# Kernel tuning notes

Measured on AMD Instinct MI355X. Metric: run time of the kernel, lower is better.

## Reference

```python
import jax, jax.numpy as jnp
import numpy as np
import math

NP, MNP, BS, DIM, NH, TOPK, FF = 512, 4096, 8, 256, 8, 32, 2048
HD = DIM // NH
EPS = 1e-5


def _ln(x, w, b):
    mu = jnp.mean(x, axis=-1, keepdims=True)
    var = jnp.mean((x - mu) ** 2, axis=-1, keepdims=True)
    return (x - mu) / jnp.sqrt(var + EPS) * w + b


def _lin(x, w, b):
    return x @ w.T + b


def setup_inputs() -> dict:
    key = jax.random.key(0)
    ks = jax.random.split(key, 16)
    s = 0.02
    d = {
        "tgt": jax.random.normal(ks[0], (NP, BS, DIM), jnp.float32),
        "memory": jax.random.normal(ks[1], (MNP, BS, DIM), jnp.float32),
        "query_pos": jax.random.normal(ks[2], (NP, BS, DIM), jnp.float32),
        "key_pos": jax.random.normal(ks[3], (MNP, BS, DIM), jnp.float32),
        "cw1": jax.random.normal(ks[4], (DIM, DIM), jnp.float32) * s,
        "cb1": jnp.zeros((DIM,), jnp.float32),
        "cw2": jax.random.normal(ks[5], (DIM, DIM), jnp.float32) * s,
        "cb2": jnp.zeros((DIM,), jnp.float32),
        "cw3": jax.random.normal(ks[6], (DIM, DIM), jnp.float32) * s,
        "cb3": jnp.zeros((DIM,), jnp.float32),
        "sa_in_w": jax.random.normal(ks[7], (3 * DIM, DIM), jnp.float32) * s,
        "sa_in_b": jnp.zeros((3 * DIM,), jnp.float32),
        "sa_out_w": jax.random.normal(ks[8], (DIM, DIM), jnp.float32) * s,
        "sa_out_b": jnp.zeros((DIM,), jnp.float32),
        "ln1_w": jnp.ones((DIM,), jnp.float32),
        "ln1_b": jnp.zeros((DIM,), jnp.float32),
        "ln2_w": jnp.ones((DIM,), jnp.float32),
        "ln2_b": jnp.zeros((DIM,), jnp.float32),
        "ln3_w": jnp.ones((DIM,), jnp.float32),
        "ln3_b": jnp.zeros((DIM,), jnp.float32),
        "ff1_w": jax.random.normal(ks[9], (FF, DIM), jnp.float32) * s,
        "ff1_b": jnp.zeros((FF,), jnp.float32),
        "ff2_w": jax.random.normal(ks[10], (DIM, FF), jnp.float32) * s,
        "ff2_b": jnp.zeros((DIM,), jnp.float32),
    }
    return d


def _forward(tgt, memory, query_pos, key_pos,
             cw1, cb1, cw2, cb2, cw3, cb3,
             sa_in_w, sa_in_b, sa_out_w, sa_out_b,
             ln1_w, ln1_b, ln2_w, ln2_b, ln3_w, ln3_b,
             ff1_w, ff1_b, ff2_w, ff2_b):
    npq, bs, dim = tgt.shape
    mnp = memory.shape[0]
    scale = 1.0 / math.sqrt(HD)

    # --- top-k cosine similarity neighbor selection (indices, non-diff) ---
    x = tgt.transpose(1, 0, 2)        # [bs, np, dim]
    m = memory.transpose(1, 0, 2)     # [bs, mnp, dim]
    xn = x / jnp.linalg.norm(x, axis=2, keepdims=True)
    mn = m / jnp.linalg.norm(m, axis=2, keepdims=True)
    sim = jnp.einsum('bnd,bmd->bnm', xn, mn)          # [bs, np, mnp]
    _, rns = jax.lax.top_k(sim, TOPK)                  # [bs, np, topk]

    # --- masked cross attention ---
    qc = (tgt + query_pos).transpose(1, 0, 2)          # [bs, np, dim]
    kc = (memory + key_pos).transpose(1, 0, 2)         # [bs, mnp, dim]
    vc = m
    qh = _lin(qc, cw1, cb1).reshape(bs, npq, NH, HD).transpose(0, 2, 1, 3)   # [bs,nh,np,hd]
    kh = _lin(kc, cw2, cb2).reshape(bs, mnp, NH, HD).transpose(0, 2, 1, 3)   # [bs,nh,mnp,hd]
    vh = _lin(vc, cw3, cb3).reshape(bs, mnp, NH, HD).transpose(0, 2, 1, 3)   # [bs,nh,mnp,hd]
    w = jnp.einsum('bhnd,bhmd->bhnm', qh, kh) * scale                         # [bs,nh,np,mnp]

    b_idx = jnp.arange(bs)[:, None, None]
    n_idx = jnp.arange(npq)[None, :, None]
    mask = jnp.zeros((bs, npq, mnp), w.dtype).at[b_idx, n_idx, rns].set(1.0)  # same for all heads
    mask = mask[:, None, :, :]                                                # [bs,1,np,mnp]
    w = w * mask + (-1e9) * (1.0 - mask)
    w = jax.nn.softmax(w, axis=3)
    cross = jnp.einsum('bhnm,bhmd->bhnd', w, vh).transpose(2, 0, 1, 3).reshape(npq, bs, dim)

    t = _ln(tgt + cross, ln1_w, ln1_b)

    # --- self attention (torch nn.MultiheadAttention, q=k=t+pos, v=t) ---
    wq, wk, wv = sa_in_w[:DIM], sa_in_w[DIM:2 * DIM], sa_in_w[2 * DIM:]
    bq, bk, bv = sa_in_b[:DIM], sa_in_b[DIM:2 * DIM], sa_in_b[2 * DIM:]
    qk = t + query_pos                                 # [np, bs, dim]
    q2 = _lin(qk, wq, bq).transpose(1, 0, 2).reshape(bs, npq, NH, HD).transpose(0, 2, 1, 3)
    k2 = _lin(qk, wk, bk).transpose(1, 0, 2).reshape(bs, npq, NH, HD).transpose(0, 2, 1, 3)
    v2 = _lin(t, wv, bv).transpose(1, 0, 2).reshape(bs, npq, NH, HD).transpose(0, 2, 1, 3)
    attn = jax.nn.softmax(jnp.einsum('bhnd,bhmd->bhnm', q2, k2) * scale, axis=-1)
    sa = jnp.einsum('bhnm,bhmd->bhnd', attn, v2).transpose(2, 0, 1, 3).reshape(npq, bs, dim)
    sa = _lin(sa, sa_out_w, sa_out_b)

    t = _ln(t + sa, ln2_w, ln2_b)

    # --- FFN (exact GELU, matching torch F.gelu default) ---
    ff = _lin(jax.nn.gelu(_lin(t, ff1_w, ff1_b), approximate=False), ff2_w, ff2_b)
    t = _ln(t + ff, ln3_w, ln3_b)
    return t


def reference(tgt, memory, query_pos, key_pos,
              cw1, cb1, cw2, cb2, cw3, cb3,
              sa_in_w, sa_in_b, sa_out_w, sa_out_b,
              ln1_w, ln1_b, ln2_w, ln2_b, ln3_w, ln3_b,
              ff1_w, ff1_b, ff2_w, ff2_b):
    return _forward(tgt, memory, query_pos, key_pos,
                    cw1, cb1, cw2, cb2, cw3, cb3,
                    sa_in_w, sa_in_b, sa_out_w, sa_out_b,
                    ln1_w, ln1_b, ln2_w, ln2_b, ln3_w, ln3_b,
                    ff1_w, ff1_b, ff2_w, ff2_b)
```

## Files before the change

### kernel.cpp

```cpp
#include <hip/hip_runtime.h>
#include <math.h>

typedef unsigned short u16;
typedef unsigned int u32;
typedef __bf16 bf16x8 __attribute__((ext_vector_type(8)));
typedef float f32x4 __attribute__((ext_vector_type(4)));

#define NPQ 512
#define MNP 4096
#define BSZ 8
#define DIM 256
#define NH 8
#define HD 32
#define TOPK 32
#define FFD 2048
#define SCALE 0.17677669529663687f

__device__ __forceinline__ u16 f2bf(float f){
  u32 u = __builtin_bit_cast(u32, f);
  u = (u + 0x7FFFu + ((u >> 16) & 1u)) >> 16;
  return (u16)u;
}
__device__ __forceinline__ float bf2f(u16 h){
  u32 u = ((u32)h) << 16;
  return __builtin_bit_cast(float, u);
}
__device__ __forceinline__ float wredsum(float v){
#pragma unroll
  for (int m = 32; m; m >>= 1) v += __shfl_xor(v, m, 64);
  return v;
}
__device__ __forceinline__ int wredsumi(int v){
#pragma unroll
  for (int m = 32; m; m >>= 1) v += __shfl_xor(v, m, 64);
  return v;
}
__device__ __forceinline__ float gelu_exact(float x){
  return 0.5f * x * (1.0f + erff(x * 0.70710678118654752f));
}

__global__ __launch_bounds__(256)
void cvt_all(const float* __restrict__ s0, const float* __restrict__ s1,
             const float* __restrict__ s2, const float* __restrict__ s3,
             const float* __restrict__ s4, const float* __restrict__ s5,
             const float* __restrict__ s6, u16* __restrict__ dst){
  int i = blockIdx.x*256 + threadIdx.x;
  if (i >= 1507328) return;
  const float* s; int base;
  if      (i <  65536){ s = s0; base = 0; }
  else if (i < 131072){ s = s1; base = 65536; }
  else if (i < 196608){ s = s2; base = 131072; }
  else if (i < 393216){ s = s3; base = 196608; }
  else if (i < 458752){ s = s4; base = 393216; }
  else if (i < 983040){ s = s5; base = 458752; }
  else                { s = s6; base = 983040; }
  dst[i] = f2bf(s[i - base]);
}

__global__ __launch_bounds__(256)
void prep_tgt(const float* __restrict__ tgt, const float* __restrict__ qpos,
              u16* __restrict__ xnh, u16* __restrict__ xnl, u16* __restrict__ qc,
              const float* __restrict__ cb2, const float* __restrict__ cb3,
              float* __restrict__ cbKV){
  __shared__ float sc[4];
  int r = blockIdx.x, t = threadIdx.x;
  if (r == 0){ cbKV[t] = cb2[t]; cbKV[256 + t] = cb3[t]; }
  int b = r >> 9, n = r & 511;
  long src = ((long)n*BSZ + b)*DIM + t;
  float x = tgt[src];
  float s = wredsum(x*x);
  if ((t & 63) == 0) sc[t >> 6] = s;
  __syncthreads();
  float tot = sc[0]+sc[1]+sc[2]+sc[3];
  float xn = x / sqrtf(tot);
  u16 hi = f2bf(xn);
  long dst = (long)r*DIM + t;
  xnh[dst] = hi;
  xnl[dst] = f2bf(xn - bf2f(hi));
  qc[dst]  = f2bf(x + qpos[src]);
}

__global__ __launch_bounds__(256)
void prep_mem(const float* __restrict__ mem, const float* __restrict__ kpos,
              u16* __restrict__ mnh, u16* __restrict__ mnl,
              u16* __restrict__ kc, u16* __restrict__ vc){
  __shared__ float sc[4];
  int r = blockIdx.x, t = threadIdx.x;
  int b = r >> 12, mp = r & 4095;
  long src = ((long)mp*BSZ + b)*DIM + t;
  float x = mem[src];
  float s = wredsum(x*x);
  if ((t & 63) == 0) sc[t >> 6] = s;
  __syncthreads();
  float tot = sc[0]+sc[1]+sc[2]+sc[3];
  float xn = x / sqrtf(tot);
  u16 hi = f2bf(xn);
  long dst = (long)r*DIM + t;
  mnh[dst] = hi;
  mnl[dst] = f2bf(xn - bf2f(hi));
  kc[dst]  = f2bf(x + kpos[src]);
  vc[dst]  = f2bf(x);
}

#define BST 136
__global__ __launch_bounds__(256, 2)
void sim_gemm(const u16* __restrict__ xnh, const u16* __restrict__ xnl,
              const u16* __restrict__ mnh, const u16* __restrict__ mnl,
              float* __restrict__ sim){
  __shared__ __align__(16) u16 Bh[128*BST];
  __shared__ __align__(16) u16 Bl[128*BST];
  int t = threadIdx.x, lane = t & 63, wv = t >> 6;
  int ml = lane & 15, quad = lane >> 4;
  int b = blockIdx.z;
  int tM = blockIdx.x * 128 + (wv & 1) * 64;
  int tN = blockIdx.y * 128;
  int nloc = (wv >> 1) * 64;
  const u16* Ah = xnh + ((long)b*NPQ + tM + ml)*DIM;
  const u16* Al = xnl + ((long)b*NPQ + tM + ml)*DIM;
  f32x4 acc[4][4];
  f32x4 zer = {0.f,0.f,0.f,0.f};
#pragma unroll
  for (int i = 0; i < 4; i++)
#pragma unroll
    for (int j = 0; j < 4; j++) acc[i][j] = zer;

  int srow = t >> 4, scg = t & 15;
  for (int half = 0; half < 2; half++){
    int k0 = half * 128;
    if (half) __syncthreads();
#pragma unroll
    for (int p = 0; p < 8; p++){
      int r = p*16 + srow;
      long g = ((long)b*MNP + tN + r)*DIM + k0 + scg*8;
      *(uint4*)(&Bh[r*BST + scg*8]) = *(const uint4*)(mnh + g);
      *(uint4*)(&Bl[r*BST + scg*8]) = *(const uint4*)(mnl + g);
    }
    __syncthreads();
#pragma unroll
    for (int kk = 0; kk < 128; kk += 32){
      bf16x8 a[4], a2[4], bh[4], bl[4];
#pragma unroll
      for (int i = 0; i < 4; i++){
        a[i]  = *(const bf16x8*)(Ah + (long)i*16*DIM + k0 + kk + quad*8);
        a2[i] = *(const bf16x8*)(Al + (long)i*16*DIM + k0 + kk + quad*8);
      }
#pragma unroll
      for (int j = 0; j < 4; j++){
        int nr = nloc + j*16 + ml;
        bh[j] = *(const bf16x8*)(&Bh[nr*BST + kk + quad*8]);
        bl[j] = *(const bf16x8*)(&Bl[nr*BST + kk + quad*8]);
      }
#pragma unroll
      for (int i = 0; i < 4; i++)
#pragma unroll
        for (int j = 0; j < 4; j++){
          acc[i][j] = __builtin_amdgcn_mfma_f32_16x16x32_bf16(a[i],  bh[j], acc[i][j], 0, 0, 0);
          acc[i][j] = __builtin_amdgcn_mfma_f32_16x16x32_bf16(a[i],  bl[j], acc[i][j], 0, 0, 0);
          acc[i][j] = __builtin_amdgcn_mfma_f32_16x16x32_bf16(a2[i], bh[j], acc[i][j], 0, 0, 0);
        }
    }
  }
  long zC = (long)b * NPQ * MNP;
#pragma unroll
  for (int i = 0; i < 4; i++)
#pragma unroll
    for (int r = 0; r < 4; r++){
      int row = tM + i*16 + quad*4 + r;
#pragma unroll
      for (int j = 0; j < 4; j++){
        int col = tN + nloc + j*16 + ml;
        sim[zC + (long)row*MNP + col] = acc[i][j][r];
      }
    }
}

#define PBST 264
template<int KGROUPS, int OUT_BF16, int ACT>
__global__ __launch_bounds__(256)
void pgemm(const u16* __restrict__ A, const u16* __restrict__ A2, int selCol,
           const u16* __restrict__ B, const float* __restrict__ bias,
           void* __restrict__ Cv, int N){
  __shared__ __align__(16) u16 Bs[64*PBST];
  const int K = KGROUPS*256;
  int t = threadIdx.x, lane = t & 63, wv = t >> 6;
  int ml = lane & 15, quad = lane >> 4;
  int tM = blockIdx.x*64;
  int tN = blockIdx.y*64;
  const u16* Ab = (tN < selCol) ? A : A2;
  const u16* Arow = Ab + (long)(tM + wv*16 + ml)*K;
  f32x4 acc[4];
  f32x4 zer = {0.f,0.f,0.f,0.f};
#pragma unroll
  for (int nj = 0; nj < 4; nj++) acc[nj] = zer;
  int srow = t >> 5, scol = (t & 31)*8;
  for (int g = 0; g < KGROUPS; g++){
    if (g) __syncthreads();
#pragma unroll
    for (int p = 0; p < 8; p++){
      int r = p*8 + srow;
      *(uint4*)(&Bs[r*PBST + scol]) = *(const uint4*)(B + (long)(tN + r)*K + g*256 + scol);
    }
    bf16x8 a[8];
#pragma unroll
    for (int kk = 0; kk < 8; kk++)
      a[kk] = *(const bf16x8*)(Arow + g*256 + kk*32 + quad*8);
    __syncthreads();
#pragma unroll
    for (int kk = 0; kk < 8; kk++){
#pragma unroll
      for (int nj = 0; nj < 4; nj++){
        bf16x8 bv = *(const bf16x8*)(&Bs[(nj*16 + ml)*PBST + kk*32 + quad*8]);
        acc[nj] = __builtin_amdgcn_mfma_f32_16x16x32_bf16(a[kk], bv, acc[nj], 0, 0, 0);
      }
    }
  }
#pragma unroll
  for (int nj = 0; nj < 4; nj++){
    int col = tN + nj*16 + ml;
    float bv = bias[col];
#pragma unroll
    for (int r = 0; r < 4; r++){
      int row = tM + wv*16 + quad*4 + r;
      float v = acc[nj][r] + bv;
      if (ACT == 1) v = gelu_exact(v);
      long idx = (long)row * N + col;
      if (OUT_BF16) ((u16*)Cv)[idx] = f2bf(v);
      else ((float*)Cv)[idx] = v;
    }
  }
}

__global__ __launch_bounds__(256)
void topk_k(const float* __restrict__ sim, int* __restrict__ rns){
  __shared__ int red[2][4];
  __shared__ int ties[64];
  __shared__ int tcnt, ocnt;
  int r = blockIdx.x, t = threadIdx.x;
  int lane = t & 63, wv = t >> 6;
  const float* row = sim + (long)r * 4096;
  u32 key[16];
#pragma unroll
  for (int i = 0; i < 16; i++){
    u32 u = __builtin_bit_cast(u32, row[i*256 + t]);
    key[i] = u ^ (((u32)((int)u >> 31)) | 0x80000000u);
  }
  if (t == 0){ tcnt = 0; ocnt = 0; }
  u32 pref = 0;
  for (int bit = 31; bit >= 0; bit--){
    u32 cand = pref | (1u << bit);
    int c = 0;
#pragma unroll
    for (int i = 0; i < 16; i++) c += (key[i] >= cand) ? 1 : 0;
    c = wredsumi(c);
    int p = bit & 1;
    if (lane == 0) red[p][wv] = c;
    __syncthreads();
    int tot = red[p][0] + red[p][1] + red[p][2] + red[p][3];
    if (tot >= TOPK) pref = cand;
  }
  int cg = 0;
#pragma unroll
  for (int i = 0; i < 16; i++) cg += (key[i] > pref) ? 1 : 0;
  cg = wredsumi(cg);
  if (lane == 0) red[0][wv] = cg;
  __syncthreads();
  int ngt = red[0][0] + red[0][1] + red[0][2] + red[0][3];
  int k_rem = TOPK - ngt;
  int* out = rns + (long)r * 32;
#pragma unroll
  for (int i = 0; i < 16; i++){
    if (key[i] > pref){
      int p = atomicAdd(&ocnt, 1);
      out[p] = i*256 + t;
    } else if (key[i] == pref){
      int p = atomicAdd(&tcnt, 1);
      if (p < 64) ties[p] = i*256 + t;
    }
  }
  __syncthreads();
  if (t == 0){
    int n = tcnt < 64 ? tcnt : 64;
    for (int s = 0; s < k_rem; s++){
      int mb = 0;
      for (int j = 1; j < n; j++) if (ties[j] < ties[mb]) mb = j;
      out[ngt + s] = ties[mb];
      ties[mb] = 0x7FFFFFFF;
    }
  }
}

#define CAS 270
__global__ __launch_bounds__(256)
void cross_attn(const u16* __restrict__ qh, const u16* __restrict__ khvh,
                const int* __restrict__ rns, float* __restrict__ crossO){
  __shared__ u16 Kg[32*CAS];
  __shared__ u16 Vg[32*CAS];
  __shared__ float qv[256];
  __shared__ int idxs[32];
  __shared__ float L[256];
  __shared__ float pm[8], ps[8];
  int r = blockIdx.x, t = threadIdx.x;
  int b = r >> 9;
  if (t < 32) idxs[t] = rns[(long)r*32 + t];
  qv[t] = bf2f(qh[(long)r*DIM + t]);
  __syncthreads();
  for (int i = t; i < 32*DIM; i += 256){
    int k = i >> 8, d = i & 255;
    long src = ((long)b*MNP + idxs[k])*512 + d;
    Kg[k*CAS + d] = khvh[src];
    Vg[k*CAS + d] = khvh[src + 256];
  }
  __syncthreads();
  {
    int h = t >> 5, k = t & 31;
    float acc = 0.f;
#pragma unroll
    for (int d = 0; d < 32; d++) acc += qv[h*HD + d] * bf2f(Kg[k*CAS + h*HD + d]);
    L[t] = acc * SCALE;
  }
  __syncthreads();
  if (t < 8){
    float m = L[t*32];
    for (int k = 1; k < 32; k++) m = fmaxf(m, L[t*32 + k]);
    float s = 0.f;
    for (int k = 0; k < 32; k++) s += expf(L[t*32 + k] - m);
    pm[t] = m; ps[t] = s;
  }
  __syncthreads();
  {
    int h = t >> 5, dd = t & 31;
    float m = pm[h], inv = 1.0f/ps[h], acc = 0.f;
#pragma unroll
    for (int k = 0; k < 32; k++) acc += expf(L[h*32 + k] - m) * bf2f(Vg[k*CAS + h*HD + dd]);
    crossO[(long)r*DIM + t] = acc * inv;
  }
}

template<int MODE>
__global__ __launch_bounds__(256)
void ln_k(const float* __restrict__ xa, const float* __restrict__ xb,
          const float* __restrict__ qpos,
          const float* __restrict__ w, const float* __restrict__ bsh,
          float* __restrict__ yf, u16* __restrict__ yb, u16* __restrict__ qkb){
  __shared__ float sc[8];
  int r = blockIdx.x, t = threadIdx.x;
  int b = r >> 9, n = r & 511;
  long bidx = (long)r*DIM + t;
  long nidx = ((long)n*BSZ + b)*DIM + t;
  float x = (MODE == 1 ? xa[nidx] : xa[bidx]) + xb[bidx];
  float s  = wredsum(x);
  float s2 = wredsum(x*x);
  int wv = t >> 6;
  if ((t & 63) == 0){ sc[wv] = s; sc[4 + wv] = s2; }
  __syncthreads();
  float S  = sc[0]+sc[1]+sc[2]+sc[3];
  float S2 = sc[4]+sc[5]+sc[6]+sc[7];
  float mu  = S * (1.f/256.f);
  float var = S2 * (1.f/256.f) - mu*mu;
  float y = (x - mu) * (1.0f / sqrtf(var + 1e-5f)) * w[t] + bsh[t];
  if (MODE == 3){
    yf[nidx] = y;
  } else {
    yf[bidx] = y;
    yb[bidx] = f2bf(y);
    if (MODE == 1) qkb[bidx] = f2bf(y + qpos[nidx]);
  }
}

#define KST 40
#define PST 264
__global__ __launch_bounds__(256)
void self_attn(const u16* __restrict__ qkv, u16* __restrict__ sa_pre){
  __shared__ __align__(16) u16 KS[512*KST];
  __shared__ __align__(16) u16 QS[32*KST];
  __shared__ float mbuf[128];
  __shared__ float sbuf[128];
  u16* P  = KS;
  u16* Vt = KS + 32*PST;

  int qt = blockIdx.x, h = blockIdx.y, b = blockIdx.z;
  int t = threadIdx.x, lane = t & 63, wv = t >> 6;
  int ml = lane & 15, quad = lane >> 4;
  int n0 = qt * 32;

  {
    int q = t >> 3, d4 = (t & 7) * 4;
    const u16* src = qkv + ((long)b*NPQ + n0 + q)*768 + h*HD + d4;
    *(ushort2*)(QS + q*KST + d4)     = *(const ushort2*)(src);
    *(ushort2*)(QS + q*KST + d4 + 2) = *(const ushort2*)(src + 2);
  }
  for (int i = t; i < 512*8; i += 256){
    int j = i >> 3, d4 = (i & 7) * 4;
    const u16* src = qkv + ((long)b*NPQ + j)*768 + 256 + h*HD + d4;
    *(ushort2*)(KS + j*KST + d4)     = *(const ushort2*)(src);
    *(ushort2*)(KS + j*KST + d4 + 2) = *(const ushort2*)(src + 2);
  }
  __syncthreads();

  f32x4 acc[2][8];
  {
    bf16x8 aq[2];
#pragma unroll
    for (int mi = 0; mi < 2; mi++)
      aq[mi] = *(const bf16x8*)(QS + (mi*16 + ml)*KST + quad*8);
#pragma unroll
    for (int nj = 0; nj < 8; nj++){
      bf16x8 bk = *(const bf16x8*)(KS + (wv*128 + nj*16 + ml)*KST + quad*8);
      f32x4 z = {0.f,0.f,0.f,0.f};
#pragma unroll
      for (int mi = 0; mi < 2; mi++)
        acc[mi][nj] = __builtin_amdgcn_mfma_f32_16x16x32_bf16(aq[mi], bk, z, 0, 0, 0);
    }
  }
  float lmax[2][4];
#pragma unroll
  for (int mi = 0; mi < 2; mi++)
#pragma unroll
    for (int r = 0; r < 4; r++) lmax[mi][r] = -3.4e38f;
#pragma unroll
  for (int mi = 0; mi < 2; mi++)
#pragma unroll
    for (int nj = 0; nj < 8; nj++)
#pragma unroll
      for (int r = 0; r < 4; r++){
        float v = acc[mi][nj][r] * SCALE;
        acc[mi][nj][r] = v;
        lmax[mi][r] = fmaxf(lmax[mi][r], v);
      }
#pragma unroll
  for (int m = 1; m < 16; m <<= 1)
#pragma unroll
    for (int mi = 0; mi < 2; mi++)
#pragma unroll
      for (int r = 0; r < 4; r++)
        lmax[mi][r] = fmaxf(lmax[mi][r], __shfl_xor(lmax[mi][r], m, 64));
  if (ml == 0){
#pragma unroll
    for (int mi = 0; mi < 2; mi++)
#pragma unroll
      for (int r = 0; r < 4; r++)
        mbuf[(mi*16 + quad*4 + r)*4 + wv] = lmax[mi][r];
  }
  __syncthreads();
  float inv_[2][4];
  float lsum[2][4];
#pragma unroll
  for (int mi = 0; mi < 2; mi++)
#pragma unroll
    for (int r = 0; r < 4; r++){
      int row = mi*16 + quad*4 + r;
      float m0 = fmaxf(fmaxf(mbuf[row*4+0], mbuf[row*4+1]),
                       fmaxf(mbuf[row*4+2], mbuf[row*4+3]));
      float s = 0.f;
#pragma unroll
      for (int nj = 0; nj < 8; nj++){
        float e = __expf(acc[mi][nj][r] - m0);
        acc[mi][nj][r] = e;
        s += e;
      }
      lsum[mi][r] = s;
    }
#pragma unroll
  for (int m = 1; m < 16; m <<= 1)
#pragma unroll
    for (int mi = 0; mi < 2; mi++)
#pragma unroll
      for (int r = 0; r < 4; r++)
        lsum[mi][r] += __shfl_xor(lsum[mi][r], m, 64);
  if (ml == 0){
#pragma unroll
    for (int mi = 0; mi < 2; mi++)
#pragma unroll
      for (int r = 0; r < 4; r++)
        sbuf[(mi*16 + quad*4 + r)*4 + wv] = lsum[mi][r];
  }
  __syncthreads();
#pragma unroll
  for (int mi = 0; mi < 2; mi++)
#pragma unroll
    for (int r = 0; r < 4; r++){
      int row = mi*16 + quad*4 + r;
      inv_[mi][r] = 1.0f / (sbuf[row*4+0]+sbuf[row*4+1]+sbuf[row*4+2]+sbuf[row*4+3]);
    }

  int mi2 = wv >> 1, ni = wv & 1;
  f32x4 acc2 = {0.f,0.f,0.f,0.f};
  for (int half = 0; half < 2; half++){
    __syncthreads();
    if ((wv >> 1) == half){
      int cbase = (wv & 1) * 128;
#pragma unroll
      for (int mi = 0; mi < 2; mi++)
#pragma unroll
        for (int nj = 0; nj < 8; nj++)
#pragma unroll
          for (int r = 0; r < 4; r++)
            P[(mi*16 + quad*4 + r)*PST + cbase + nj*16 + ml] = f2bf(acc[mi][nj][r]);
    }
    for (int i = t; i < 2048; i += 256){
      int j = i >> 3, d4 = (i & 7) * 4;
      const u16* src = qkv + ((long)b*NPQ + half*256 + j)*768 + 512 + h*HD + d4;
      u16 v0 = src[0], v1 = src[1], v2e = src[2], v3 = src[3];
      Vt[(d4+0)*PST + j] = v0;
      Vt[(d4+1)*PST + j] = v1;
      Vt[(d4+2)*PST + j] = v2e;
      Vt[(d4+3)*PST + j] = v3;
    }
    __syncthreads();
#pragma unroll
    for (int k0 = 0; k0 < 256; k0 += 32){
      bf16x8 ap = *(const bf16x8*)(P  + (mi2*16 + ml)*PST + k0 + quad*8);
      bf16x8 bv = *(const bf16x8*)(Vt + (ni*16  + ml)*PST + k0 + quad*8);
      acc2 = __builtin_amdgcn_mfma_f32_16x16x32_bf16(ap, bv, acc2, 0, 0, 0);
    }
  }
#pragma unroll
  for (int r = 0; r < 4; r++){
    int row = mi2*16 + quad*4 + r;
    sa_pre[((long)b*NPQ + n0 + row)*DIM + h*HD + ni*16 + ml] =
        f2bf(acc2[r] * inv_[mi2][r]);
  }
}

extern "C" void kernel_launch(void* const* d_in, const int* in_sizes, int n_in,
                              void* d_out, int out_size, void* d_ws, size_t ws_size,
                              hipStream_t stream){
  (void)in_sizes; (void)n_in; (void)out_size; (void)ws_size;
  const float* tgt  = (const float*)d_in[0];
  const float* mem  = (const float*)d_in[1];
  const float* qpos = (const float*)d_in[2];
  const float* kpos = (const float*)d_in[3];
  const float* cw1  = (const float*)d_in[4];  const float* cb1 = (const float*)d_in[5];
  const float* cw2  = (const float*)d_in[6];  const float* cb2 = (const float*)d_in[7];
  const float* cw3  = (const float*)d_in[8];  const float* cb3 = (const float*)d_in[9];
  const float* saw  = (const float*)d_in[10]; const float* sab = (const float*)d_in[11];
  const float* sow  = (const float*)d_in[12]; const float* sob = (const float*)d_in[13];
  const float* ln1w = (const float*)d_in[14]; const float* ln1b = (const float*)d_in[15];
  const float* ln2w = (const float*)d_in[16]; const float* ln2b = (const float*)d_in[17];
  const float* ln3w = (const float*)d_in[18]; const float* ln3b = (const float*)d_in[19];
  const float* f1w  = (const float*)d_in[20]; const float* f1bs = (const float*)d_in[21];
  const float* f2w  = (const float*)d_in[22]; const float* f2bs = (const float*)d_in[23];

  char* base = (char*)d_ws;
  size_t off = 0;
  auto alloc = [&](size_t bytes) -> char* {
    char* p = base + off;
    off += (bytes + 255) & ~(size_t)255;
    return p;
  };
  u16* cw1b = (u16*)alloc(65536u*2);
  u16* cw2b = (u16*)alloc(65536u*2);
  u16* cw3b = (u16*)alloc(65536u*2);   (void)cw3b;
  u16* sawb = (u16*)alloc(196608u*2);
  u16* sowb = (u16*)alloc(65536u*2);
  u16* f1wb = (u16*)alloc(524288u*2);
  u16* f2wb = (u16*)alloc(524288u*2);
  int* rns  = (int*)alloc(4096u*32*4);
  float* cbKV = (float*)alloc(512*4);
  size_t offB = off;
  u16* xnh = (u16*)alloc((size_t)4096*256*2);
  u16* xnl = (u16*)alloc((size_t)4096*256*2);
  u16* mnh = (u16*)alloc((size_t)32768*256*2);
  u16* mnl = (u16*)alloc((size_t)32768*256*2);
  u16* qc  = (u16*)alloc((size_t)4096*256*2);
  u16* kc  = (u16*)alloc((size_t)32768*256*2);
  u16* vc  = (u16*)alloc((size_t)32768*256*2);
  float* sim = (float*)alloc((size_t)8*512*4096*4);

  char* regC = (char*)sim;
  u16* qh   = (u16*)regC;
  u16* khvh = (u16*)(regC + 2097152);
  char* regB = base + offB;
  size_t ob = 0;
  auto allocB = [&](size_t bytes) -> char* {
    char* p = regB + ob;
    ob += (bytes + 255) & ~(size_t)255;
    return p;
  };
  float* cross = (float*)allocB((size_t)4096*256*4);
  float* t1    = (float*)allocB((size_t)4096*256*4);
  u16*   t1b   = (u16*)allocB((size_t)4096*256*2);
  u16*   qkb   = (u16*)allocB((size_t)4096*256*2);
  u16*   qkv   = (u16*)allocB((size_t)4096*768*2);
  u16*   sa_pre= (u16*)allocB((size_t)4096*256*2);
  float* sa    = (float*)allocB((size_t)4096*256*4);
  float* t2    = (float*)allocB((size_t)4096*256*4);
  u16*   t2b   = (u16*)allocB((size_t)4096*256*2);
  u16*   h1    = (u16*)allocB((size_t)4096*2048*2);
  float* ff    = (float*)allocB((size_t)4096*256*4);

  const int BIG = 1 << 30;
  dim3 blk(256);
  cvt_all<<<dim3((1507328 + 255)/256), blk, 0, stream>>>(
      cw1, cw2, cw3, saw, sow, f1w, f2w, cw1b);
  prep_tgt<<<dim3(4096), blk, 0, stream>>>(tgt, qpos, xnh, xnl, qc, cb2, cb3, cbKV);
  prep_mem<<<dim3(32768), blk, 0, stream>>>(mem, kpos, mnh, mnl, kc, vc);
  sim_gemm<<<dim3(4,32,8), blk, 0, stream>>>(xnh, xnl, mnh, mnl, sim);
  topk_k<<<dim3(4096), blk, 0, stream>>>(sim, rns);
  pgemm<1,1,0><<<dim3(64,4), blk, 0, stream>>>(qc, qc, BIG, cw1b, cb1, qh, 256);
  pgemm<1,1,0><<<dim3(512,8), blk, 0, stream>>>(kc, vc, 256, cw2b, cbKV, khvh, 512);
  cross_attn<<<dim3(4096), blk, 0, stream>>>(qh, khvh, rns, cross);
  ln_k<1><<<dim3(4096), blk, 0, stream>>>(tgt, cross, qpos, ln1w, ln1b, t1, t1b, qkb);
  pgemm<1,1,0><<<dim3(64,12), blk, 0, stream>>>(qkb, t1b, 512, sawb, sab, qkv, 768);
  self_attn<<<dim3(16,8,8), blk, 0, stream>>>(qkv, sa_pre);
  pgemm<1,0,0><<<dim3(64,4), blk, 0, stream>>>(sa_pre, sa_pre, BIG, sowb, sob, sa, 256);
  ln_k<2><<<dim3(4096), blk, 0, stream>>>(t1, sa, nullptr, ln2w, ln2b, t2, t2b, nullptr);
  pgemm<1,1,1><<<dim3(64,32), blk, 0, stream>>>(t2b, t2b, BIG, f1wb, f1bs, h1, 2048);
  pgemm<8,0,0><<<dim3(64,4), blk, 0, stream>>>(h1, h1, BIG, f2wb, f2bs, ff, 256);
  ln_k<3><<<dim3(4096), blk, 0, stream>>>(t2, ff, nullptr, ln3w, ln3b, (float*)d_out, nullptr, nullptr);
}
```

Measured before the change: 452.9 us.

## Rework top-k to one wave per row, prefetch sim A-operands, vectorize cross-attn gathers

The top-k kernel now gives each row to a single 64-lane wave. Counting is done with ballot and popcount instead of a block-wide shared-memory reduction with a barrier on every bit, which removes 32 __syncthreads per row and reads the row with 16-byte loads. The similarity GEMM swaps its grid axes and software-prefetches the next k-slice of A-operands from global memory into registers, to overlap load latency with MFMA work. The cross-attention gather now copies K/V rows with 4-element vector loads into 16-byte-aligned padded shared memory. Holding 64 keys per lane raises register pressure in top-k, and the prefetch adds registers to the GEMM.

```diff
diff --git a/kernel.cpp b/kernel.cpp
--- a/kernel.cpp
+++ b/kernel.cpp
@@ -30,13 +30,11 @@
   for (int m = 32; m; m >>= 1) v += __shfl_xor(v, m, 64);
   return v;
 }
-__device__ __forceinline__ int wredsumi(int v){
-#pragma unroll
-  for (int m = 32; m; m >>= 1) v += __shfl_xor(v, m, 64);
-  return v;
-}
 __device__ __forceinline__ float gelu_exact(float x){
   return 0.5f * x * (1.0f + erff(x * 0.70710678118654752f));
+}
+__device__ __forceinline__ u32 keytr(u32 u){
+  return u ^ (((u32)((int)u >> 31)) | 0x80000000u);
 }
 
 __global__ __launch_bounds__(256)
@@ -112,8 +110,8 @@
   int t = threadIdx.x, lane = t & 63, wv = t >> 6;
   int ml = lane & 15, quad = lane >> 4;
   int b = blockIdx.z;
-  int tM = blockIdx.x * 128 + (wv & 1) * 64;
-  int tN = blockIdx.y * 128;
+  int tM = blockIdx.y * 128 + (wv & 1) * 64;
+  int tN = blockIdx.x * 128;
   int nloc = (wv >> 1) * 64;
   const u16* Ah = xnh + ((long)b*NPQ + tM + ml)*DIM;
   const u16* Al = xnl + ((long)b*NPQ + tM + ml)*DIM;
@@ -135,15 +133,23 @@
       *(uint4*)(&Bh[r*BST + scg*8]) = *(const uint4*)(mnh + g);
       *(uint4*)(&Bl[r*BST + scg*8]) = *(const uint4*)(mnl + g);
     }
+    bf16x8 ca[4], ca2[4], na[4], na2[4];
+#pragma unroll
+    for (int i = 0; i < 4; i++){
+      ca[i]  = *(const bf16x8*)(Ah + (long)i*16*DIM + k0 + quad*8);
+      ca2[i] = *(const bf16x8*)(Al + (long)i*16*DIM + k0 + quad*8);
+    }
     __syncthreads();
 #pragma unroll
     for (int kk = 0; kk < 128; kk += 32){
-      bf16x8 a[4], a2[4], bh[4], bl[4];
-#pragma unroll
-      for (int i = 0; i < 4; i++){
-        a[i]  = *(const bf16x8*)(Ah + (long)i*16*DIM + k0 + kk + quad*8);
-        a2[i] = *(const bf16x8*)(Al + (long)i*16*DIM + k0 + kk + quad*8);
+      if (kk < 96){
+#pragma unroll
+        for (int i = 0; i < 4; i++){
+          na[i]  = *(const bf16x8*)(Ah + (long)i*16*DIM + k0 + kk + 32 + quad*8);
+          na2[i] = *(const bf16x8*)(Al + (long)i*16*DIM + k0 + kk + 32 + quad*8);
+        }
       }
+      bf16x8 bh[4], bl[4];
 #pragma unroll
       for (int j = 0; j < 4; j++){
         int nr = nloc + j*16 + ml;
@@ -154,10 +160,12 @@
       for (int i = 0; i < 4; i++)
 #pragma unroll
         for (int j = 0; j < 4; j++){
-          acc[i][j] = __builtin_amdgcn_mfma_f32_16x16x32_bf16(a[i],  bh[j], acc[i][j], 0, 0, 0);
-          acc[i][j] = __builtin_amdgcn_mfma_f32_16x16x32_bf16(a[i],  bl[j], acc[i][j], 0, 0, 0);
-          acc[i][j] = __builtin_amdgcn_mfma_f32_16x16x32_bf16(a2[i], bh[j], acc[i][j], 0, 0, 0);
+          acc[i][j] = __builtin_amdgcn_mfma_f32_16x16x32_bf16(ca[i],  bh[j], acc[i][j], 0, 0, 0);
+          acc[i][j] = __builtin_amdgcn_mfma_f32_16x16x32_bf16(ca[i],  bl[j], acc[i][j], 0, 0, 0);
+          acc[i][j] = __builtin_amdgcn_mfma_f32_16x16x32_bf16(ca2[i], bh[j], acc[i][j], 0, 0, 0);
         }
+#pragma unroll
+      for (int i = 0; i < 4; i++){ ca[i] = na[i]; ca2[i] = na2[i]; }
     }
   }
   long zC = (long)b * NPQ * MNP;
@@ -232,69 +240,66 @@
 
 __global__ __launch_bounds__(256)
 void topk_k(const float* __restrict__ sim, int* __restrict__ rns){
-  __shared__ int red[2][4];
-  __shared__ int ties[64];
-  __shared__ int tcnt, ocnt;
-  int r = blockIdx.x, t = threadIdx.x;
-  int lane = t & 63, wv = t >> 6;
-  const float* row = sim + (long)r * 4096;
-  u32 key[16];
-#pragma unroll
-  for (int i = 0; i < 16; i++){
-    u32 u = __builtin_bit_cast(u32, row[i*256 + t]);
-    key[i] = u ^ (((u32)((int)u >> 31)) | 0x80000000u);
-  }
-  if (t == 0){ tcnt = 0; ocnt = 0; }
+  __shared__ int scnt[4];
+  __shared__ int stcnt[4];
+  __shared__ int sties[4][64];
+  int t = threadIdx.x, lane = t & 63, wv = t >> 6;
+  int r = blockIdx.x*4 + wv;
+  const uint4* row4 = (const uint4*)(sim + (long)r * 4096);
+  u32 key[64];
+#pragma unroll
+  for (int j = 0; j < 16; j++){
+    uint4 v = row4[j*64 + lane];
+    key[j*4+0] = keytr(v.x);
+    key[j*4+1] = keytr(v.y);
+    key[j*4+2] = keytr(v.z);
+    key[j*4+3] = keytr(v.w);
+  }
+  if (lane == 0){ scnt[wv] = 0; stcnt[wv] = 0; }
   u32 pref = 0;
+#pragma unroll 1
   for (int bit = 31; bit >= 0; bit--){
     u32 cand = pref | (1u << bit);
-    int c = 0;
-#pragma unroll
-    for (int i = 0; i < 16; i++) c += (key[i] >= cand) ? 1 : 0;
-    c = wredsumi(c);
-    int p = bit & 1;
-    if (lane == 0) red[p][wv] = c;
-    __syncthreads();
-    int tot = red[p][0] + red[p][1] + red[p][2] + red[p][3];
-    if (tot >= TOPK) pref = cand;
+    int cnt = 0;
+#pragma unroll
+    for (int i = 0; i < 64; i++)
+      cnt += (int)__popcll(__ballot(key[i] >= cand));
+    if (cnt >= TOPK) pref = cand;
   }
   int cg = 0;
 #pragma unroll
-  for (int i = 0; i < 16; i++) cg += (key[i] > pref) ? 1 : 0;
-  cg = wredsumi(cg);
-  if (lane == 0) red[0][wv] = cg;
-  __syncthreads();
-  int ngt = red[0][0] + red[0][1] + red[0][2] + red[0][3];
-  int k_rem = TOPK - ngt;
+  for (int i = 0; i < 64; i++)
+    cg += (int)__popcll(__ballot(key[i] > pref));
+  int k_rem = TOPK - cg;
   int* out = rns + (long)r * 32;
 #pragma unroll
-  for (int i = 0; i < 16; i++){
+  for (int i = 0; i < 64; i++){
+    int gidx = (i >> 2)*256 + lane*4 + (i & 3);
     if (key[i] > pref){
-      int p = atomicAdd(&ocnt, 1);
-      out[p] = i*256 + t;
+      int p = atomicAdd(&scnt[wv], 1);
+      out[p] = gidx;
     } else if (key[i] == pref){
-      int p = atomicAdd(&tcnt, 1);
-      if (p < 64) ties[p] = i*256 + t;
-    }
-  }
-  __syncthreads();
-  if (t == 0){
-    int n = tcnt < 64 ? tcnt : 64;
+      int p = atomicAdd(&stcnt[wv], 1);
+      if (p < 64) sties[wv][p] = gidx;
+    }
+  }
+  if (lane == 0){
+    int n = stcnt[wv]; if (n > 64) n = 64;
     for (int s = 0; s < k_rem; s++){
       int mb = 0;
-      for (int j = 1; j < n; j++) if (ties[j] < ties[mb]) mb = j;
-      out[ngt + s] = ties[mb];
-      ties[mb] = 0x7FFFFFFF;
-    }
-  }
-}
-
-#define CAS 270
+      for (int j = 1; j < n; j++) if (sties[wv][j] < sties[wv][mb]) mb = j;
+      out[cg + s] = sties[wv][mb];
+      sties[wv][mb] = 0x7FFFFFFF;
+    }
+  }
+}
+
+#define CAS 272
 __global__ __launch_bounds__(256)
 void cross_attn(const u16* __restrict__ qh, const u16* __restrict__ khvh,
                 const int* __restrict__ rns, float* __restrict__ crossO){
-  __shared__ u16 Kg[32*CAS];
-  __shared__ u16 Vg[32*CAS];
+  __shared__ __align__(16) u16 Kg[32*CAS];
+  __shared__ __align__(16) u16 Vg[32*CAS];
   __shared__ float qv[256];
   __shared__ int idxs[32];
   __shared__ float L[256];
@@ -304,11 +309,11 @@
   if (t < 32) idxs[t] = rns[(long)r*32 + t];
   qv[t] = bf2f(qh[(long)r*DIM + t]);
   __syncthreads();
-  for (int i = t; i < 32*DIM; i += 256){
-    int k = i >> 8, d = i & 255;
-    long src = ((long)b*MNP + idxs[k])*512 + d;
-    Kg[k*CAS + d] = khvh[src];
-    Vg[k*CAS + d] = khvh[src + 256];
+  for (int i = t; i < 32*64; i += 256){
+    int k = i >> 6, c = (i & 63) * 4;
+    long src = ((long)b*MNP + idxs[k])*512 + c;
+    *(ushort4*)(&Kg[k*CAS + c]) = *(const ushort4*)(khvh + src);
+    *(ushort4*)(&Vg[k*CAS + c]) = *(const ushort4*)(khvh + src + 256);
   }
   __syncthreads();
   {
@@ -595,8 +600,8 @@
       cw1, cw2, cw3, saw, sow, f1w, f2w, cw1b);
   prep_tgt<<<dim3(4096), blk, 0, stream>>>(tgt, qpos, xnh, xnl, qc, cb2, cb3, cbKV);
   prep_mem<<<dim3(32768), blk, 0, stream>>>(mem, kpos, mnh, mnl, kc, vc);
-  sim_gemm<<<dim3(4,32,8), blk, 0, stream>>>(xnh, xnl, mnh, mnl, sim);
-  topk_k<<<dim3(4096), blk, 0, stream>>>(sim, rns);
+  sim_gemm<<<dim3(32,4,8), blk, 0, stream>>>(xnh, xnl, mnh, mnl, sim);
+  topk_k<<<dim3(1024), blk, 0, stream>>>(sim, rns);
   pgemm<1,1,0><<<dim3(64,4), blk, 0, stream>>>(qc, qc, BIG, cw1b, cb1, qh, 256);
   pgemm<1,1,0><<<dim3(512,8), blk, 0, stream>>>(kc, vc, 256, cw2b, cbKV, khvh, 512);
   cross_attn<<<dim3(4096), blk, 0, stream>>>(qh, khvh, rns, cross);
```

Measured after the change: 447.1 us. About the same (-1.3%).
